# Kernel optimization log

Hardware: AMD Instinct MI355X
Metric: run time of the kernel (lower is better)

Reference implementation:

```python
import jax, jax.numpy as jnp
import numpy as np

CROP = 7  # feature_genetic1 crop size
NCH = 1024  # channels looped over in feature_genetic1


def _genetic(x, ih, iw):
    # x: [B, 1024, H, W]; ih, iw: [1024] per-channel random crop offsets in [0,7)
    ch = jnp.arange(NCH)
    rows = ih[:, None] + jnp.arange(CROP)          # [1024, 7]
    cols = iw[:, None] + jnp.arange(CROP)          # [1024, 7]
    # fused gather: out[b, c, i, j] = x[b, c, ih[c]+i, iw[c]+j]
    return x[:, ch[:, None, None], rows[:, :, None], cols[:, None, :]]  # [B,1024,7,7]


def _avg_pool_5s2p2(x):
    # torch F.avg_pool2d(x, 5, stride=2, padding=2), count_include_pad=True
    s = jax.lax.reduce_window(x, 0.0, jax.lax.add,
                              (1, 1, 5, 5), (1, 1, 2, 2),
                              ((0, 0), (0, 0), (2, 2), (2, 2)))
    return s / 25.0


def setup_inputs() -> dict:
    key = jax.random.key(0)
    ks = jax.random.split(key, 10)
    B = 64
    return {
        "x1": jax.random.normal(ks[0], (B, 1024, 14, 14), jnp.float32),
        "x2": jax.random.normal(ks[1], (B, 1024, 14, 14), jnp.float32),
        "x3": jax.random.normal(ks[2], (B, 1280, 28, 28), jnp.float32),
        "share_feature": jax.random.normal(ks[3], (B, 1024, 14, 14), jnp.float32),
        "c_w": jax.random.normal(ks[4], (1024, 1280), jnp.float32) * 0.02,
        "conv3d_w": jax.random.normal(ks[5], (32, 16, 3, 3, 3), jnp.float32) * 0.05,
        "lin_w": jax.random.normal(ks[6], (768, 1), jnp.float32) * 0.02,
        "lin_b": jax.random.normal(ks[7], (1,), jnp.float32),
        "idx_h": jax.random.randint(ks[8], (4, 1024), 0, 7, jnp.int32),
        "idx_w": jax.random.randint(ks[9], (4, 1024), 0, 7, jnp.int32),
    }


def reference(x1, x2, x3, share_feature, c_w, conv3d_w, lin_w, lin_b, idx_h, idx_w):
    B = x1.shape[0]
    # x3 path: avg_pool2d(5, 2, 2) -> Conv2d(1280->1024, 1x1, no bias)
    x3p = _avg_pool_5s2p2(x3)                                  # [B,1280,14,14]
    x3p = jnp.einsum('bchw,oc->bohw', x3p, c_w)                # [B,1024,14,14]
    # four per-channel random-crop gathers (the 1024-iter python loop, fused)
    g1 = _genetic(x1, idx_h[0], idx_w[0])
    g2 = _genetic(x2, idx_h[1], idx_w[1])
    g3 = _genetic(x3p, idx_h[2], idx_w[2])
    gs = _genetic(share_feature, idx_h[3], idx_w[3])
    xa = jnp.concatenate([g1, g2], axis=2)                     # [B,1024,14,7]
    xb = jnp.concatenate([g3, gs], axis=2)                     # [B,1024,14,7]
    x = jnp.concatenate([xa, xb], axis=3)                      # [B,1024,14,14]
    x = x.reshape(B, 16, 64, 14, 14)
    # Conv3d(16->32, k=3, stride=(3,1,1), pad=(4,1,1), no bias): depth 64 -> 24
    x = jax.lax.conv_general_dilated(
        x, conv3d_w, window_strides=(3, 1, 1),
        padding=((4, 4), (1, 1), (1, 1)),
        dimension_numbers=('NCDHW', 'OIDHW', 'NCDHW'))         # [B,32,24,14,14]
    x = x.reshape(B, 768, 14, 14)
    # ViT stub: global average pool; head: Linear(768 -> 1)
    x = x.mean(axis=(2, 3))                                    # [B,768]
    return x @ lin_w + lin_b                                   # [B,1]
```

## Files before the change

### kernel.cpp

```cpp
#include <hip/hip_runtime.h>

#define NCH 1024

typedef float f4v __attribute__((ext_vector_type(4)));


__global__ void k2_maps(const float* __restrict__ w3,
                        const float* __restrict__ lin_w,
                        const int* __restrict__ idx_h,
                        const int* __restrict__ idx_w,
                        float* __restrict__ A1,
                        float* __restrict__ A2,
                        float* __restrict__ As,
                        float* __restrict__ G3) {
  __shared__ float lweff[9];
  int c = blockIdx.x;
  int t = threadIdx.x;
  int dd = c & 63, ich = c >> 6;
  int kd = (dd + 4) % 3;
  int d  = (dd + 4 - kd) / 3;
  if (t < 9) {
    float acc = 0.f;
    for (int o = 0; o < 32; ++o)
      acc += lin_w[o * 24 + d] * w3[(((o * 16 + ich) * 3) + kd) * 9 + t];
    lweff[t] = acc * (1.f / 196.f);
  }
  __syncthreads();
  if (t >= 196) return;
  float weff[9];
#pragma unroll
  for (int k = 0; k < 9; ++k) weff[k] = lweff[k];
  float rh[3][3];
#pragma unroll
  for (int kw = 0; kw < 3; ++kw) {
    rh[0][kw] = weff[0 * 3 + kw] + weff[1 * 3 + kw];
    rh[1][kw] = weff[0 * 3 + kw] + weff[1 * 3 + kw] + weff[2 * 3 + kw];
    rh[2][kw] = weff[1 * 3 + kw] + weff[2 * 3 + kw];
  }
  float p[9];
#pragma unroll
  for (int hc = 0; hc < 3; ++hc) {
    p[hc * 3 + 0] = rh[hc][0] + rh[hc][1];
    p[hc * 3 + 1] = rh[hc][0] + rh[hc][1] + rh[hc][2];
    p[hc * 3 + 2] = rh[hc][1] + rh[hc][2];
  }
  int h = t / 14, w = t % 14;
  {
    int i = h - idx_h[0 * NCH + c], j = w - idx_w[0 * NCH + c];
    bool in = (i >= 0 && i < 7 && j >= 0 && j < 7);
    int hc = (i == 0) ? 0 : 1, wc = (j == 0) ? 0 : 1;
    A1[c * 196 + t] = in ? p[hc * 3 + wc] : 0.f;
  }
  {
    int i = h - idx_h[1 * NCH + c], j = w - idx_w[1 * NCH + c];
    bool in = (i >= 0 && i < 7 && j >= 0 && j < 7);
    int hc = (i == 6) ? 2 : 1, wc = (j == 0) ? 0 : 1;
    A2[c * 196 + t] = in ? p[hc * 3 + wc] : 0.f;
  }
  {
    int i = h - idx_h[3 * NCH + c], j = w - idx_w[3 * NCH + c];
    bool in = (i >= 0 && i < 7 && j >= 0 && j < 7);
    int hc = (i == 6) ? 2 : 1, wc = (j == 6) ? 2 : 1;
    As[c * 196 + t] = in ? p[hc * 3 + wc] : 0.f;
  }
  {
    int i = h - idx_h[2 * NCH + c], j = w - idx_w[2 * NCH + c];
    bool in = (i >= 0 && i < 7 && j >= 0 && j < 7);
    int hc = (i == 0) ? 0 : 1, wc = (j == 6) ? 2 : 1;
    G3[c * 196 + t] = in ? p[hc * 3 + wc] : 0.f;
  }
}

__global__ __launch_bounds__(256) void k3_vgemm(const float* __restrict__ c_w,
                                                const float* __restrict__ G3,
                                                float* __restrict__ Vp) {
  __shared__ float cwT[64][64];
  __shared__ float g3t[64][64];
  int cc0 = blockIdx.x * 64;
  int p0 = blockIdx.y * 64;
  int kz = blockIdx.z;
  int tid = threadIdx.x;
  int lane = tid & 63, wid = tid >> 6;
  int tc = lane & 15;
  int pq = wid * 4 + (lane >> 4);
  float acc[4][4];
#pragma unroll
  for (int i = 0; i < 4; ++i)
#pragma unroll
    for (int j = 0; j < 4; ++j) acc[i][j] = 0.f;
  for (int k0 = kz * 128; k0 < kz * 128 + 128; k0 += 64) {
#pragma unroll
    for (int r = 0; r < 4; ++r) {
      int idx4 = r * 256 + tid;
      int kk = idx4 >> 4, c4 = idx4 & 15;
      *(float4*)&cwT[kk][c4 * 4] =
          *(const float4*)&c_w[(size_t)(k0 + kk) * 1280 + cc0 + c4 * 4];
    }
#pragma unroll
    for (int r = 0; r < 4; ++r) {
      int idx4 = r * 256 + tid;
      int kk = idx4 >> 4, p4 = idx4 & 15;
      int p = p0 + p4 * 4;
      float4 v = (p < 196) ? *(const float4*)&G3[(size_t)(k0 + kk) * 196 + p]
                           : float4{0.f, 0.f, 0.f, 0.f};
      *(float4*)&g3t[kk][p4 * 4] = v;
    }
    __syncthreads();
#pragma unroll
    for (int kk = 0; kk < 64; ++kk) {
      float4 a = *(const float4*)&cwT[kk][tc * 4];
      float4 b = *(const float4*)&g3t[kk][pq * 4];
      acc[0][0] += a.x * b.x; acc[0][1] += a.x * b.y; acc[0][2] += a.x * b.z; acc[0][3] += a.x * b.w;
      acc[1][0] += a.y * b.x; acc[1][1] += a.y * b.y; acc[1][2] += a.y * b.z; acc[1][3] += a.y * b.w;
      acc[2][0] += a.z * b.x; acc[2][1] += a.z * b.y; acc[2][2] += a.z * b.z; acc[2][3] += a.z * b.w;
      acc[3][0] += a.w * b.x; acc[3][1] += a.w * b.y; acc[3][2] += a.w * b.z; acc[3][3] += a.w * b.w;
    }
    __syncthreads();
  }
  int p = p0 + pq * 4;
  if (p < 196) {
#pragma unroll
    for (int i = 0; i < 4; ++i) {
      int cc = cc0 + tc * 4 + i;
      *(float4*)&Vp[(size_t)kz * 250880 + (size_t)cc * 196 + p] =
          float4{acc[i][0], acc[i][1], acc[i][2], acc[i][3]};
    }
  }
}

__global__ void k4_unpool(const float* __restrict__ Vp, float* __restrict__ U) {
  __shared__ float v[196];
  int cc = blockIdx.x;
  int t = threadIdx.x;
  if (t < 196) {
    float s = 0.f;
#pragma unroll
    for (int z = 0; z < 8; ++z)
      s += Vp[(size_t)z * 250880 + (size_t)cc * 196 + t];
    v[t] = s;
  }
  __syncthreads();
  for (int q = t; q < 784; q += blockDim.x) {
    int H = q / 28, W = q % 28;
    int hlo = (H - 1) / 2; if (hlo < 0) hlo = 0;
    int hhi = (H + 2) / 2; if (hhi > 13) hhi = 13;
    int wlo = (W - 1) / 2; if (wlo < 0) wlo = 0;
    int whi = (W + 2) / 2; if (whi > 13) whi = 13;
    float s = 0.f;
    for (int h = hlo; h <= hhi; ++h)
      for (int w = wlo; w <= whi; ++w) s += v[h * 14 + w];
    U[(size_t)cc * 784 + q] = s * 0.04f;
  }
}

__global__ __launch_bounds__(512) void kdot(const f4v* __restrict__ x1,
                                            const f4v* __restrict__ x2,
                                            const f4v* __restrict__ xs,
                                            const f4v* __restrict__ x3,
                                            const f4v* __restrict__ A,
                                            const f4v* __restrict__ U,
                                            float* __restrict__ part) {
  __shared__ f4v lw[1024];
  int bid = blockIdx.x;
  int z, bg, cx;
  size_t stride;
  const f4v *xt, *wbase;
  if (bid < 1176) {
    z = bid / 392;
    int rr = bid % 392;
    cx = rr >> 3;
    bg = rr & 7;
    xt = (z == 0) ? x1 : (z == 1) ? x2 : xs;
    stride = 50176;
    wbase = A + (size_t)z * 50176 + (size_t)cx * 1024;
  } else {
    int rr = bid - 1176;
    z = 3;
    cx = rr >> 3;
    bg = rr & 7;
    xt = x3;
    stride = 250880;
    wbase = U + (size_t)cx * 1024;
  }
  int t = threadIdx.x;
  lw[t] = wbase[t];
  lw[512 + t] = wbase[512 + t];
  __syncthreads();
  int w = t >> 6, lane = t & 63;
  int b = bg * 8 + w;
  const f4v* xb = xt + (size_t)b * stride + (size_t)cx * 1024;
  float s = 0.f;
#pragma unroll
  for (int i = 0; i < 16; ++i) {
    f4v a = xb[i * 64 + lane];
    f4v ww = lw[i * 64 + lane];
    s += a.x * ww.x + a.y * ww.y + a.z * ww.z + a.w * ww.w;
  }
#pragma unroll
  for (int off = 32; off > 0; off >>= 1) s += __shfl_down(s, off, 64);
  if (lane == 0) part[((z * 64 + b) << 8) + cx] = s;
}

__global__ void k7_final(const float* __restrict__ part,
                         const float* __restrict__ lin_b,
                         float* __restrict__ out) {
  int b = threadIdx.x;
  if (b >= 64) return;
  float s = lin_b[0];
  for (int z = 0; z < 3; ++z)
#pragma unroll
    for (int cx = 0; cx < 49; ++cx) s += part[((z * 64 + b) << 8) + cx];
#pragma unroll
  for (int cx = 0; cx < 245; ++cx) s += part[((192 + b) << 8) + cx];
  out[b] = s;
}

extern "C" void kernel_launch(void* const* d_in, const int* in_sizes, int n_in,
                              void* d_out, int out_size, void* d_ws, size_t ws_size,
                              hipStream_t stream) {
  const float* x1 = (const float*)d_in[0];
  const float* x2 = (const float*)d_in[1];
  const float* x3 = (const float*)d_in[2];
  const float* sf = (const float*)d_in[3];
  const float* c_w = (const float*)d_in[4];
  const float* w3 = (const float*)d_in[5];
  const float* lin_w = (const float*)d_in[6];
  const float* lin_b = (const float*)d_in[7];
  const int* idx_h = (const int*)d_in[8];
  const int* idx_w = (const int*)d_in[9];
  float* out = (float*)d_out;
  float* ws = (float*)d_ws;

  float* A = ws;
  float* G3 = A + 602112;
  float* Vp = G3 + 200704;
  float* U = Vp + 2007040;
  float* part = U + 1003520;

  k2_maps<<<dim3(1024), dim3(256), 0, stream>>>(w3, lin_w, idx_h, idx_w,
                                                A, A + 200704, A + 2 * 200704, G3);
  k3_vgemm<<<dim3(20, 4, 8), dim3(256), 0, stream>>>(c_w, G3, Vp);
  k4_unpool<<<dim3(1280), dim3(256), 0, stream>>>(Vp, U);
  kdot<<<dim3(3136), dim3(512), 0, stream>>>(
      (const f4v*)x1, (const f4v*)x2, (const f4v*)sf,
      (const f4v*)x3, (const f4v*)A, (const f4v*)U, part);
  k7_final<<<dim3(1), dim3(64), 0, stream>>>(part, lin_b, out);
}
```

Baseline: 142.7 us.

## Fuse unpool into x3 dot kernel and retile dot products per channel

Drops the separate unpool kernel and its global U buffer. The upsampled 28x28 weight map is now built in shared memory inside a per-channel x3 dot kernel. The x1/x2/share dot products are split into their own kernel, where each block covers four channels across all 64 batches, so the weights are loaded once per block. The final reduction becomes 512 threads with shuffle reduction. The aim is to save the U write and read traffic and one launch; in exchange each x3 block recomputes its unpool locally, and per-thread access is narrower and strided.

```diff
diff --git a/kernel.cpp b/kernel.cpp
--- a/kernel.cpp
+++ b/kernel.cpp
@@ -128,8 +128,47 @@
   }
 }
 
-__global__ void k4_unpool(const float* __restrict__ Vp, float* __restrict__ U) {
-  __shared__ float v[196];
+__global__ __launch_bounds__(512) void kdotA(const f4v* __restrict__ x1,
+                                             const f4v* __restrict__ x2,
+                                             const f4v* __restrict__ xs,
+                                             const f4v* __restrict__ A,
+                                             float* __restrict__ part) {
+  __shared__ f4v lw[196];
+  int bid = blockIdx.x;
+  int z = bid >> 8;
+  int cq = bid & 255;
+  const f4v* xt = (z == 0) ? x1 : (z == 1) ? x2 : xs;
+  int t = threadIdx.x;
+  if (t < 196) lw[t] = A[(size_t)z * 50176 + cq * 196 + t];
+  __syncthreads();
+  int b = t >> 3, q = t & 7;
+  const f4v* xb = xt + (size_t)b * 50176 + cq * 196;
+  float s = 0.f;
+#pragma unroll
+  for (int k = 0; k < 24; ++k) {
+    int j = q + 8 * k;
+    f4v a = xb[j];
+    f4v w = lw[j];
+    s += a.x * w.x + a.y * w.y + a.z * w.z + a.w * w.w;
+  }
+  if (q < 4) {
+    int j = q + 192;
+    f4v a = xb[j];
+    f4v w = lw[j];
+    s += a.x * w.x + a.y * w.y + a.z * w.z + a.w * w.w;
+  }
+  s += __shfl_xor(s, 1, 64);
+  s += __shfl_xor(s, 2, 64);
+  s += __shfl_xor(s, 4, 64);
+  if (q == 0) part[(size_t)(z * 64 + b) * 1280 + cq] = s;
+}
+
+__global__ __launch_bounds__(512) void kdotX3(const f4v* __restrict__ x3,
+                                              const float* __restrict__ Vp,
+                                              float* __restrict__ part) {
+  __shared__ float vs[196];
+  __shared__ f4v uu4[196];
+  float* uu = (float*)uu4;
   int cc = blockIdx.x;
   int t = threadIdx.x;
   if (t < 196) {
@@ -137,82 +176,60 @@
 #pragma unroll
     for (int z = 0; z < 8; ++z)
       s += Vp[(size_t)z * 250880 + (size_t)cc * 196 + t];
-    v[t] = s;
-  }
-  __syncthreads();
-  for (int q = t; q < 784; q += blockDim.x) {
-    int H = q / 28, W = q % 28;
+    vs[t] = s;
+  }
+  __syncthreads();
+  for (int px = t; px < 784; px += 512) {
+    int H = px / 28, W = px % 28;
     int hlo = (H - 1) / 2; if (hlo < 0) hlo = 0;
     int hhi = (H + 2) / 2; if (hhi > 13) hhi = 13;
     int wlo = (W - 1) / 2; if (wlo < 0) wlo = 0;
     int whi = (W + 2) / 2; if (whi > 13) whi = 13;
     float s = 0.f;
     for (int h = hlo; h <= hhi; ++h)
-      for (int w = wlo; w <= whi; ++w) s += v[h * 14 + w];
-    U[(size_t)cc * 784 + q] = s * 0.04f;
-  }
-}
-
-__global__ __launch_bounds__(512) void kdot(const f4v* __restrict__ x1,
-                                            const f4v* __restrict__ x2,
-                                            const f4v* __restrict__ xs,
-                                            const f4v* __restrict__ x3,
-                                            const f4v* __restrict__ A,
-                                            const f4v* __restrict__ U,
-                                            float* __restrict__ part) {
-  __shared__ f4v lw[1024];
-  int bid = blockIdx.x;
-  int z, bg, cx;
-  size_t stride;
-  const f4v *xt, *wbase;
-  if (bid < 1176) {
-    z = bid / 392;
-    int rr = bid % 392;
-    cx = rr >> 3;
-    bg = rr & 7;
-    xt = (z == 0) ? x1 : (z == 1) ? x2 : xs;
-    stride = 50176;
-    wbase = A + (size_t)z * 50176 + (size_t)cx * 1024;
-  } else {
-    int rr = bid - 1176;
-    z = 3;
-    cx = rr >> 3;
-    bg = rr & 7;
-    xt = x3;
-    stride = 250880;
-    wbase = U + (size_t)cx * 1024;
-  }
-  int t = threadIdx.x;
-  lw[t] = wbase[t];
-  lw[512 + t] = wbase[512 + t];
-  __syncthreads();
-  int w = t >> 6, lane = t & 63;
-  int b = bg * 8 + w;
-  const f4v* xb = xt + (size_t)b * stride + (size_t)cx * 1024;
+      for (int w = wlo; w <= whi; ++w) s += vs[h * 14 + w];
+    uu[px] = s * 0.04f;
+  }
+  __syncthreads();
+  int b = t >> 3, q = t & 7;
+  const f4v* xb = x3 + (size_t)b * 250880 + (size_t)cc * 196;
   float s = 0.f;
 #pragma unroll
-  for (int i = 0; i < 16; ++i) {
-    f4v a = xb[i * 64 + lane];
-    f4v ww = lw[i * 64 + lane];
-    s += a.x * ww.x + a.y * ww.y + a.z * ww.z + a.w * ww.w;
-  }
-#pragma unroll
-  for (int off = 32; off > 0; off >>= 1) s += __shfl_down(s, off, 64);
-  if (lane == 0) part[((z * 64 + b) << 8) + cx] = s;
-}
-
-__global__ void k7_final(const float* __restrict__ part,
-                         const float* __restrict__ lin_b,
-                         float* __restrict__ out) {
-  int b = threadIdx.x;
-  if (b >= 64) return;
-  float s = lin_b[0];
+  for (int k = 0; k < 24; ++k) {
+    int j = q + 8 * k;
+    f4v a = xb[j];
+    f4v w = uu4[j];
+    s += a.x * w.x + a.y * w.y + a.z * w.z + a.w * w.w;
+  }
+  if (q < 4) {
+    int j = q + 192;
+    f4v a = xb[j];
+    f4v w = uu4[j];
+    s += a.x * w.x + a.y * w.y + a.z * w.z + a.w * w.w;
+  }
+  s += __shfl_xor(s, 1, 64);
+  s += __shfl_xor(s, 2, 64);
+  s += __shfl_xor(s, 4, 64);
+  if (q == 0) part[(size_t)(192 + b) * 1280 + cc] = s;
+}
+
+__global__ __launch_bounds__(512) void k7_final(const float* __restrict__ part,
+                                                const float* __restrict__ lin_b,
+                                                float* __restrict__ out) {
+  int t = threadIdx.x;
+  int b = t >> 3, q = t & 7;
+  float s = 0.f;
   for (int z = 0; z < 3; ++z)
 #pragma unroll
-    for (int cx = 0; cx < 49; ++cx) s += part[((z * 64 + b) << 8) + cx];
-#pragma unroll
-  for (int cx = 0; cx < 245; ++cx) s += part[((192 + b) << 8) + cx];
-  out[b] = s;
+    for (int k = 0; k < 32; ++k)
+      s += part[(size_t)(z * 64 + b) * 1280 + q + 8 * k];
+#pragma unroll
+  for (int k = 0; k < 160; ++k)
+    s += part[(size_t)(192 + b) * 1280 + q + 8 * k];
+  s += __shfl_xor(s, 1, 64);
+  s += __shfl_xor(s, 2, 64);
+  s += __shfl_xor(s, 4, 64);
+  if (q == 0) out[b] = s + lin_b[0];
 }
 
 extern "C" void kernel_launch(void* const* d_in, const int* in_sizes, int n_in,
@@ -234,15 +251,13 @@
   float* A = ws;
   float* G3 = A + 602112;
   float* Vp = G3 + 200704;
-  float* U = Vp + 2007040;
-  float* part = U + 1003520;
+  float* part = Vp + 2007040;
 
   k2_maps<<<dim3(1024), dim3(256), 0, stream>>>(w3, lin_w, idx_h, idx_w,
                                                 A, A + 200704, A + 2 * 200704, G3);
   k3_vgemm<<<dim3(20, 4, 8), dim3(256), 0, stream>>>(c_w, G3, Vp);
-  k4_unpool<<<dim3(1280), dim3(256), 0, stream>>>(Vp, U);
-  kdot<<<dim3(3136), dim3(512), 0, stream>>>(
-      (const f4v*)x1, (const f4v*)x2, (const f4v*)sf,
-      (const f4v*)x3, (const f4v*)A, (const f4v*)U, part);
-  k7_final<<<dim3(1), dim3(64), 0, stream>>>(part, lin_b, out);
-}
+  kdotA<<<dim3(768), dim3(512), 0, stream>>>(
+      (const f4v*)x1, (const f4v*)x2, (const f4v*)sf, (const f4v*)A, part);
+  kdotX3<<<dim3(1280), dim3(512), 0, stream>>>((const f4v*)x3, Vp, part);
+  k7_final<<<dim3(1), dim3(512), 0, stream>>>(part, lin_b, out);
+}
```

New measurement: 150.5 us. 1.05x slower.

## Restructure dot kernel to hold weights in registers across 8 batches; parallelize final reduction

Applied to the files above, without the earlier changes.

The dot-product kernel no longer stages weights in shared memory. Each thread now loads its weight vector once into registers and reuses it across 8 batch rows, keeping 8 accumulators, and a cross-wave shared reduction replaces the per-wave single-batch layout. Blocks shrink to 256 threads. The final reduction moves from one 64-thread block with serial loops to 64 blocks that each do a parallel reduction, cutting the serial tail. Register pressure rises and the x loads per thread are strided across batches.

```diff
diff --git a/kernel.cpp b/kernel.cpp
--- a/kernel.cpp
+++ b/kernel.cpp
@@ -153,18 +153,17 @@
   }
 }
 
-__global__ __launch_bounds__(512) void kdot(const f4v* __restrict__ x1,
+__global__ __launch_bounds__(256) void kdot(const f4v* __restrict__ x1,
                                             const f4v* __restrict__ x2,
                                             const f4v* __restrict__ xs,
                                             const f4v* __restrict__ x3,
                                             const f4v* __restrict__ A,
                                             const f4v* __restrict__ U,
                                             float* __restrict__ part) {
-  __shared__ f4v lw[1024];
   int bid = blockIdx.x;
   int z, bg, cx;
   size_t stride;
-  const f4v *xt, *wbase;
+  const f4v *xt, *wb;
   if (bid < 1176) {
     z = bid / 392;
     int rr = bid % 392;
@@ -172,7 +171,7 @@
     bg = rr & 7;
     xt = (z == 0) ? x1 : (z == 1) ? x2 : xs;
     stride = 50176;
-    wbase = A + (size_t)z * 50176 + (size_t)cx * 1024;
+    wb = A + (size_t)z * 50176 + (size_t)cx * 1024;
   } else {
     int rr = bid - 1176;
     z = 3;
@@ -180,39 +179,58 @@
     bg = rr & 7;
     xt = x3;
     stride = 250880;
-    wbase = U + (size_t)cx * 1024;
-  }
-  int t = threadIdx.x;
-  lw[t] = wbase[t];
-  lw[512 + t] = wbase[512 + t];
-  __syncthreads();
-  int w = t >> 6, lane = t & 63;
-  int b = bg * 8 + w;
-  const f4v* xb = xt + (size_t)b * stride + (size_t)cx * 1024;
+    wb = U + (size_t)cx * 1024;
+  }
+  int t = threadIdx.x;
+  const f4v* xb = xt + (size_t)(bg * 8) * stride + (size_t)cx * 1024;
+  float s[8];
+#pragma unroll
+  for (int b = 0; b < 8; ++b) s[b] = 0.f;
+#pragma unroll
+  for (int u = 0; u < 4; ++u) {
+    f4v w = wb[u * 256 + t];
+#pragma unroll
+    for (int b = 0; b < 8; ++b) {
+      f4v a = xb[(size_t)b * stride + u * 256 + t];
+      s[b] += a.x * w.x + a.y * w.y + a.z * w.z + a.w * w.w;
+    }
+  }
+  int lane = t & 63, wid = t >> 6;
+  __shared__ float red[8][4];
+#pragma unroll
+  for (int b = 0; b < 8; ++b) {
+    float v = s[b];
+#pragma unroll
+    for (int off = 32; off > 0; off >>= 1) v += __shfl_down(v, off, 64);
+    if (lane == 0) red[b][wid] = v;
+  }
+  __syncthreads();
+  if (t < 8) {
+    float r4 = red[t][0] + red[t][1] + red[t][2] + red[t][3];
+    int row = z * 64 + bg * 8 + t;
+    part[(row << 8) + cx] = r4;
+  }
+}
+
+__global__ __launch_bounds__(256) void k7_final(const float* __restrict__ part,
+                                                const float* __restrict__ lin_b,
+                                                float* __restrict__ out) {
+  int b = blockIdx.x;
+  int t = threadIdx.x;
   float s = 0.f;
-#pragma unroll
-  for (int i = 0; i < 16; ++i) {
-    f4v a = xb[i * 64 + lane];
-    f4v ww = lw[i * 64 + lane];
-    s += a.x * ww.x + a.y * ww.y + a.z * ww.z + a.w * ww.w;
-  }
+  if (t < 49) {
+    s += part[((0 * 64 + b) << 8) + t];
+    s += part[((1 * 64 + b) << 8) + t];
+    s += part[((2 * 64 + b) << 8) + t];
+  }
+  if (t < 245) s += part[((3 * 64 + b) << 8) + t];
 #pragma unroll
   for (int off = 32; off > 0; off >>= 1) s += __shfl_down(s, off, 64);
-  if (lane == 0) part[((z * 64 + b) << 8) + cx] = s;
-}
-
-__global__ void k7_final(const float* __restrict__ part,
-                         const float* __restrict__ lin_b,
-                         float* __restrict__ out) {
-  int b = threadIdx.x;
-  if (b >= 64) return;
-  float s = lin_b[0];
-  for (int z = 0; z < 3; ++z)
-#pragma unroll
-    for (int cx = 0; cx < 49; ++cx) s += part[((z * 64 + b) << 8) + cx];
-#pragma unroll
-  for (int cx = 0; cx < 245; ++cx) s += part[((192 + b) << 8) + cx];
-  out[b] = s;
+  __shared__ float red[4];
+  int lane = t & 63, wid = t >> 6;
+  if (lane == 0) red[wid] = s;
+  __syncthreads();
+  if (t == 0) out[b] = red[0] + red[1] + red[2] + red[3] + lin_b[0];
 }
 
 extern "C" void kernel_launch(void* const* d_in, const int* in_sizes, int n_in,
@@ -241,8 +259,8 @@
                                                 A, A + 200704, A + 2 * 200704, G3);
   k3_vgemm<<<dim3(20, 4, 8), dim3(256), 0, stream>>>(c_w, G3, Vp);
   k4_unpool<<<dim3(1280), dim3(256), 0, stream>>>(Vp, U);
-  kdot<<<dim3(3136), dim3(512), 0, stream>>>(
+  kdot<<<dim3(3136), dim3(256), 0, stream>>>(
       (const f4v*)x1, (const f4v*)x2, (const f4v*)sf,
       (const f4v*)x3, (const f4v*)A, (const f4v*)U, part);
-  k7_final<<<dim3(1), dim3(64), 0, stream>>>(part, lin_b, out);
-}
+  k7_final<<<dim3(64), dim3(256), 0, stream>>>(part, lin_b, out);
+}
```

After: 139.5 us. 2.3% less time.

## Restructure dot-product kernel to per-batch blocks and parallelise final reduction

Applied to the files above, without the earlier changes.

The dot kernel now assigns each 256-thread block one batch row and a long contiguous slice of channels. Weights are read directly from global memory instead of being staged in shared memory for 8 batches. Partial sums are reduced across waves in shared memory and written to a compact partial array. The final kernel uses one block per batch element with a wave shuffle reduction instead of a single serial thread loop. This trades weight reuse through LDS for longer streaming loops and less final-reduction latency, relying on L2 for repeated weight reads.

```diff
diff --git a/kernel.cpp b/kernel.cpp
--- a/kernel.cpp
+++ b/kernel.cpp
@@ -153,66 +153,66 @@
   }
 }
 
-__global__ __launch_bounds__(512) void kdot(const f4v* __restrict__ x1,
+__global__ __launch_bounds__(256) void kdot(const f4v* __restrict__ x1,
                                             const f4v* __restrict__ x2,
                                             const f4v* __restrict__ xs,
                                             const f4v* __restrict__ x3,
                                             const f4v* __restrict__ A,
                                             const f4v* __restrict__ U,
                                             float* __restrict__ part) {
-  __shared__ f4v lw[1024];
   int bid = blockIdx.x;
-  int z, bg, cx;
-  size_t stride;
-  const f4v *xt, *wbase;
-  if (bid < 1176) {
-    z = bid / 392;
-    int rr = bid % 392;
-    cx = rr >> 3;
-    bg = rr & 7;
-    xt = (z == 0) ? x1 : (z == 1) ? x2 : xs;
-    stride = 50176;
-    wbase = A + (size_t)z * 50176 + (size_t)cx * 1024;
+  int t = threadIdx.x;
+  const f4v *xp, *wp;
+  int niter, row, col;
+  if (bid < 1344) {
+    int zy = bid / 7;
+    int bx = bid % 7;
+    int z = zy >> 6, b = zy & 63;
+    const f4v* xt = (z == 0) ? x1 : (z == 1) ? x2 : xs;
+    xp = xt + (size_t)b * 50176 + (size_t)bx * 7168 + t;
+    wp = A + (size_t)z * 50176 + (size_t)bx * 7168 + t;
+    niter = 28;
+    row = zy; col = bx;
   } else {
-    int rr = bid - 1176;
-    z = 3;
-    cx = rr >> 3;
-    bg = rr & 7;
-    xt = x3;
-    stride = 250880;
-    wbase = U + (size_t)cx * 1024;
-  }
-  int t = threadIdx.x;
-  lw[t] = wbase[t];
-  lw[512 + t] = wbase[512 + t];
+    int r = bid - 1344;
+    int b = r / 28;
+    int bx = r % 28;
+    xp = x3 + (size_t)b * 250880 + (size_t)bx * 8960 + t;
+    wp = U + (size_t)bx * 8960 + t;
+    niter = 35;
+    row = 192 + b; col = bx;
+  }
+  float s = 0.f;
+#pragma unroll 7
+  for (int k = 0; k < niter; ++k) {
+    f4v a = xp[k * 256];
+    f4v w = wp[k * 256];
+    s += a.x * w.x + a.y * w.y + a.z * w.z + a.w * w.w;
+  }
+#pragma unroll
+  for (int off = 32; off > 0; off >>= 1) s += __shfl_down(s, off, 64);
+  __shared__ float red[4];
+  int lane = t & 63, wid = t >> 6;
+  if (lane == 0) red[wid] = s;
   __syncthreads();
-  int w = t >> 6, lane = t & 63;
-  int b = bg * 8 + w;
-  const f4v* xb = xt + (size_t)b * stride + (size_t)cx * 1024;
+  if (t == 0) part[row * 32 + col] = red[0] + red[1] + red[2] + red[3];
+}
+
+__global__ __launch_bounds__(64) void k7_final(const float* __restrict__ part,
+                                               const float* __restrict__ lin_b,
+                                               float* __restrict__ out) {
+  int b = blockIdx.x;
+  int j = threadIdx.x;
   float s = 0.f;
-#pragma unroll
-  for (int i = 0; i < 16; ++i) {
-    f4v a = xb[i * 64 + lane];
-    f4v ww = lw[i * 64 + lane];
-    s += a.x * ww.x + a.y * ww.y + a.z * ww.z + a.w * ww.w;
+  if (j < 21) {
+    int z = j / 7, bx = j % 7;
+    s = part[(z * 64 + b) * 32 + bx];
+  } else if (j < 49) {
+    s = part[(192 + b) * 32 + (j - 21)];
   }
 #pragma unroll
   for (int off = 32; off > 0; off >>= 1) s += __shfl_down(s, off, 64);
-  if (lane == 0) part[((z * 64 + b) << 8) + cx] = s;
-}
-
-__global__ void k7_final(const float* __restrict__ part,
-                         const float* __restrict__ lin_b,
-                         float* __restrict__ out) {
-  int b = threadIdx.x;
-  if (b >= 64) return;
-  float s = lin_b[0];
-  for (int z = 0; z < 3; ++z)
-#pragma unroll
-    for (int cx = 0; cx < 49; ++cx) s += part[((z * 64 + b) << 8) + cx];
-#pragma unroll
-  for (int cx = 0; cx < 245; ++cx) s += part[((192 + b) << 8) + cx];
-  out[b] = s;
+  if (j == 0) out[b] = s + lin_b[0];
 }
 
 extern "C" void kernel_launch(void* const* d_in, const int* in_sizes, int n_in,
@@ -241,8 +241,8 @@
                                                 A, A + 200704, A + 2 * 200704, G3);
   k3_vgemm<<<dim3(20, 4, 8), dim3(256), 0, stream>>>(c_w, G3, Vp);
   k4_unpool<<<dim3(1280), dim3(256), 0, stream>>>(Vp, U);
-  kdot<<<dim3(3136), dim3(512), 0, stream>>>(
+  kdot<<<dim3(3136), dim3(256), 0, stream>>>(
       (const f4v*)x1, (const f4v*)x2, (const f4v*)sf,
       (const f4v*)x3, (const f4v*)A, (const f4v*)U, part);
-  k7_final<<<dim3(1), dim3(64), 0, stream>>>(part, lin_b, out);
-}
+  k7_final<<<dim3(64), dim3(64), 0, stream>>>(part, lin_b, out);
+}
```

Result: no change. 145.1 us (+1.6%).
